# Performance work log

Hardware: AMD Instinct MI355X
Metric: run time of the kernel (lower is better)

## Reference

```python
import jax, jax.numpy as jnp
import numpy as np

# Module hyperparameters (init_kwargs)
NH = 254          # nHidden
NSTEP = 32        # MPC horizon
DT = 1.0 / 60.0   # del_t
EPS = 1e-4
PQ = 5.0
QV = 200.0
QA = 1.0
N_STATE = NH + 2  # hidden embedding + [position, velocity]
NBATCH = 256


def setup_inputs() -> dict:
    key = jax.random.key(0)
    k1, k2, k3, k4, k5, k6 = jax.random.split(key, 6)
    x = jax.random.normal(k1, (NBATCH, NH), dtype=jnp.float32)
    gripper_p = jax.random.normal(k2, (NBATCH,), dtype=jnp.float32)
    own_gripper_v = jax.random.normal(k3, (NBATCH,), dtype=jnp.float32)
    other_gripper_v = jax.random.normal(k4, (NBATCH,), dtype=jnp.float32)
    # Learned parameters (as in __init__): Af ~ U[0,1), Lq = tril(U[0,1))
    Af = jax.random.uniform(k5, (NH, 1), dtype=jnp.float32)
    Lq = jnp.tril(jax.random.uniform(k6, (NH, NH), dtype=jnp.float32))
    return {"x": x, "gripper_p": gripper_p, "own_gripper_v": own_gripper_v,
            "other_gripper_v": other_gripper_v, "Af": Af, "Lq": Lq}


def _mpc_forward(x, gripper_p, own_gripper_v, Af, Lq):
    n = N_STATE
    dt = x.dtype
    eye_n = jnp.eye(n, dtype=dt)

    # ---- Q0: [[Lq Lq^T + eps I, 0], [0, diag(0, Qv)]]  (n x n) ----
    Q0_tl = Lq @ Lq.T + EPS * jnp.eye(NH, dtype=dt)
    Q0 = jnp.zeros((n, n), dt).at[:NH, :NH].set(Q0_tl).at[NH + 1, NH + 1].set(QV)
    w = jnp.ones((NSTEP,), dt).at[-1].set(PQ)        # final-step weight Pq
    Q0_stack = w[:, None, None] * Q0                 # [NSTEP, n, n]
    Q_dia = jax.scipy.linalg.block_diag(*Q0_stack)   # [NSTEP*n, NSTEP*n]

    # ---- A0: [[I, 0, Af], [0, 1, dt], [0, 0, 1]] ----
    A0 = jnp.zeros((n, n), dt)
    A0 = A0.at[:NH, :NH].set(jnp.eye(NH, dtype=dt)).at[:NH, NH + 1].set(Af[:, 0])
    A0 = A0.at[NH, NH].set(1.0).at[NH, NH + 1].set(DT).at[NH + 1, NH + 1].set(1.0)

    # ---- powers A0^1..A0^NSTEP via scan (replaces the Python power loop) ----
    def step(carry, _):
        nxt = carry @ A0
        return nxt, nxt
    _, Pk = jax.lax.scan(step, eye_n, None, length=NSTEP)   # Pk[k] = A0^{k+1}
    P = jnp.concatenate([eye_n[None], Pk], axis=0)          # A0^0 .. A0^NSTEP
    T_ = Pk.reshape(NSTEP * n, n)                           # vstack(A0^1..A0^NSTEP)

    # ---- AN_: block lower-triangular Toeplitz, block (i,j) = A0^{i-j} for j<=i ----
    d = jnp.arange(NSTEP)[:, None] - jnp.arange(NSTEP)[None, :]
    blocks = jnp.where((d >= 0)[:, :, None, None],
                       P[jnp.clip(d, 0, NSTEP)], jnp.zeros((), dt))  # [NSTEP,NSTEP,n,n]
    AN_ = blocks.transpose(0, 2, 1, 3).reshape(NSTEP * n, NSTEP * n)

    B0 = jnp.zeros((n, 1), dt).at[NH, 0].set(0.5 * DT * DT).at[NH + 1, 0].set(DT)
    B_dia = jax.scipy.linalg.block_diag(*jnp.broadcast_to(B0, (NSTEP, n, 1)))

    S_ = AN_ @ B_dia                                        # [NSTEP*n, NSTEP]
    QS = Q_dia @ S_                                         # [NSTEP*n, NSTEP]
    Q_final = 2.0 * (QA * jnp.eye(NSTEP, dtype=dt) + S_.T @ QS) \
              + EPS * jnp.eye(NSTEP, dtype=dt)
    p_final = 2.0 * (T_.T @ QS)                             # [n, NSTEP]

    # ---- batch state x0 = [x, gripper_p, own_gripper_v] ----
    x0 = jnp.concatenate([x, gripper_p[:, None], own_gripper_v[:, None]], axis=1)
    p_x0 = x0 @ p_final                                     # [B, NSTEP]

    # QPFunction with G=0, h=0, no equalities -> unconstrained QP:
    # u = argmin 0.5 u^T Q_final u + p_x0^T u = -Q_final^{-1} p_x0
    u = -jnp.linalg.solve(Q_final, p_x0.T).T                # [B, NSTEP]

    # x_predict = S u + T x0 ; output picks position component (index NH) per step
    x_pred = u @ S_.T + x0 @ T_.T                           # [B, NSTEP*n]
    posi = x_pred.reshape(-1, NSTEP, n)[:, :, NH]           # [B, NSTEP]
    return posi


def reference(x, gripper_p, own_gripper_v, other_gripper_v, Af, Lq):
    # other_gripper_v is accepted but unused in the active forward path (as in source)
    return _mpc_forward(x, gripper_p, own_gripper_v, Af, Lq)
```

## Files before the change

kernel.cpp:

```cpp
#include <hip/hip_runtime.h>

#define NH 254
#define NSTEP 32
#define NB 256

constexpr float  FEPS = 1e-4f;
constexpr double DDT  = 1.0 / 60.0;
constexpr double DQV  = 200.0;
constexpr double DPQ  = 5.0;
constexpr double DQA  = 1.0;
constexpr double DEPS = 1e-4;

__global__ __launch_bounds__(256) void k_fused(const float* __restrict__ Lq,
                                               const float* __restrict__ Af,
                                               const float* __restrict__ x,
                                               const float* __restrict__ gp,
                                               const float* __restrict__ gv,
                                               float* __restrict__ out) {
    __shared__ float  af_sh[256];
    __shared__ float  x_sh[256];
    __shared__ float  t_sh[256];
    __shared__ float  svals[4];
    __shared__ double red[4];
    __shared__ double M[32][34];
    __shared__ double ua[32], ub[32];
    __shared__ float  cA[32], cB[32];

    const int b    = blockIdx.x;
    const int tid  = threadIdx.x;
    const int lane = tid & 63;
    const int wv   = tid >> 6;

    const float gpv = gp[b];
    const float gvv = gv[b];

    af_sh[tid] = (tid < NH) ? Af[tid] : 0.f;
    x_sh[tid]  = (tid < NH) ? x[b * NH + tid] : 0.f;
    __syncthreads();

    {
        float acc = 0.f;
        if (tid < NH) {
            for (int i0 = (tid & ~31); i0 < NH; i0 += 32) {
                float v[32];
                #pragma unroll
                for (int j = 0; j < 32; ++j) {
                    const int i = i0 + j;
                    v[j] = (i < NH) ? Lq[i * NH + tid] : 0.f;
                }
                #pragma unroll
                for (int j = 0; j < 32; ++j)
                    acc += v[j] * af_sh[i0 + j];
            }
        }
        t_sh[tid] = acc;
    }
    __syncthreads();

    {
        float sacc = 0.f;
        for (int r = 0; r < 64; r += 4) {
            float a4[4] = {0.f, 0.f, 0.f, 0.f};
            #pragma unroll
            for (int rr = 0; rr < 4; ++rr) {
                const int i = 64 * wv + r + rr;
                #pragma unroll
                for (int c = 0; c < 4; ++c) {
                    const int kk = lane + 64 * c;
                    const float lv = (i < NH && kk < NH) ? Lq[i * NH + kk] : 0.f;
                    a4[rr] += lv * t_sh[kk];
                }
            }
            #pragma unroll
            for (int rr = 0; rr < 4; ++rr) {
                #pragma unroll
                for (int off = 32; off; off >>= 1)
                    a4[rr] += __shfl_xor(a4[rr], off, 64);
            }
            #pragma unroll
            for (int rr = 0; rr < 4; ++rr) {
                const int i = 64 * wv + r + rr;
                sacc += x_sh[i] * (a4[rr] + FEPS * af_sh[i]);
            }
        }
        if (lane == 0) svals[wv] = sacc;
    }

    {
        double dv = 0.0;
        if (tid < NH) {
            const double td = (double)t_sh[tid];
            const double ad = (double)af_sh[tid];
            dv = td * td + DEPS * ad * ad;
        }
        #pragma unroll
        for (int off = 32; off; off >>= 1) dv += __shfl_xor(dv, off, 64);
        if (lane == 0) red[wv] = dv;
    }
    __syncthreads();
    const double c = red[0] + red[1] + red[2] + red[3];

    for (int e = tid; e < 1024; e += 256) {
        const int j1 = e >> 5, j2 = e & 31;
        const int m = (j1 > j2) ? j1 : j2;
        double s = 0.0;
        for (int kk = m; kk < 32; ++kk) {
            const double wk = (kk == 31) ? DPQ : 1.0;
            s += wk * ((double)(kk - j1) * (double)(kk - j2) * c + DQV);
        }
        M[j1][j2] = 2.0 * DDT * DDT * s + ((j1 == j2) ? (2.0 * DQA + DEPS) : 0.0);
    }
    if (tid < 32) {
        const int j = tid;
        double sa = 0.0, sb = 0.0;
        for (int kk = j; kk < 32; ++kk) {
            const double wk = (kk == 31) ? DPQ : 1.0;
            sa += wk * (double)(kk - j);
            sb += wk * ((double)(kk + 1) * (double)(kk - j) * c + DQV);
        }
        M[j][32] = 2.0 * DDT * sa;
        M[j][33] = 2.0 * DDT * sb;
    }
    __syncthreads();

    {
        const int r   = tid & 31;
        const int cg8 = tid >> 5;
        for (int p = 0; p < 32; ++p) {
            const double f = M[r][p] / M[p][p];
            if (r != p) {
                for (int cc = cg8; cc < 34; cc += 8)
                    if (cc > p) M[r][cc] -= f * M[p][cc];
            }
            __syncthreads();
        }
    }
    if (tid < 32) {
        ua[tid] = -M[tid][32] / M[tid][tid];
        ub[tid] = -M[tid][33] / M[tid][tid];
    }
    __syncthreads();
    if (tid < 32) {
        const int i = tid;
        double ca = 0.0, cb = 0.0;
        for (int j = 0; j <= i; ++j) {
            const double wgt = (double)(i - j) + 0.5;
            ca += wgt * ua[j];
            cb += wgt * ub[j];
        }
        cA[i] = (float)(ca * DDT * DDT);
        cB[i] = (float)((double)(i + 1) * DDT + cb * DDT * DDT);
    }
    __syncthreads();

    if (tid < 32) {
        const float s = svals[0] + svals[1] + svals[2] + svals[3];
        out[b * NSTEP + tid] = gpv + gvv * cB[tid] + s * cA[tid];
    }
}

extern "C" void kernel_launch(void* const* d_in, const int* in_sizes, int n_in,
                              void* d_out, int out_size, void* d_ws, size_t ws_size,
                              hipStream_t stream) {
    const float* x  = (const float*)d_in[0];
    const float* gp = (const float*)d_in[1];
    const float* gv = (const float*)d_in[2];
    const float* Af = (const float*)d_in[4];
    const float* Lq = (const float*)d_in[5];
    float* out = (float*)d_out;

    k_fused<<<NB, 256, 0, stream>>>(Lq, Af, x, gp, gv, out);
}
```

Measured before the change: 106.8 us.

## Split fused kernel into batched Lq^T x product, single solve, and output kernels

The single fused kernel made every batch block recompute t = Lq^T Af and redo the 32x32 double-precision elimination. Now one kernel computes Y = Lq^T x for four batch rows per block (plus t once), one single-block kernel does the solve, and a small kernel combines the results. This removes the per-block duplicate work on Lq and the solve, but adds two kernel launches and a round trip of Y and t through a workspace.

```diff
diff --git a/kernel.cpp b/kernel.cpp
--- a/kernel.cpp
+++ b/kernel.cpp
@@ -11,86 +11,68 @@
 constexpr double DQA  = 1.0;
 constexpr double DEPS = 1e-4;
 
-__global__ __launch_bounds__(256) void k_fused(const float* __restrict__ Lq,
+__global__ __launch_bounds__(256) void k_yt(const float* __restrict__ Lq,
+                                            const float* __restrict__ Af,
+                                            const float* __restrict__ x,
+                                            float* __restrict__ Y,
+                                            float* __restrict__ t_out) {
+    __shared__ float af_sh[256];
+    __shared__ float x_sh[4][256];
+    const int k = threadIdx.x;
+    const int b = blockIdx.x;
+
+    af_sh[k] = (k < NH) ? Af[k] : 0.f;
+    #pragma unroll
+    for (int r = 0; r < 4; ++r) {
+        const int row = 4 * b + r;
+        x_sh[r][k] = (k < NH) ? x[row * NH + k] : 0.f;
+    }
+    __syncthreads();
+
+    float ty = 0.f;
+    float y0 = 0.f, y1 = 0.f, y2 = 0.f, y3 = 0.f;
+    if (k < NH) {
+        for (int i0 = (k & ~31); i0 < NH; i0 += 32) {
+            float v[32];
+            #pragma unroll
+            for (int j = 0; j < 32; ++j) {
+                const int i = i0 + j;
+                v[j] = (i < NH) ? Lq[i * NH + k] : 0.f;
+            }
+            #pragma unroll
+            for (int j = 0; j < 32; ++j) {
+                const int i = i0 + j;
+                ty += v[j] * af_sh[i];
+                y0 += v[j] * x_sh[0][i];
+                y1 += v[j] * x_sh[1][i];
+                y2 += v[j] * x_sh[2][i];
+                y3 += v[j] * x_sh[3][i];
+            }
+        }
+    }
+    Y[(4 * b + 0) * 256 + k] = y0;
+    Y[(4 * b + 1) * 256 + k] = y1;
+    Y[(4 * b + 2) * 256 + k] = y2;
+    Y[(4 * b + 3) * 256 + k] = y3;
+    if (b == 0) t_out[k] = ty;
+}
+
+__global__ __launch_bounds__(256) void k_solve(const float* __restrict__ t_in,
                                                const float* __restrict__ Af,
-                                               const float* __restrict__ x,
-                                               const float* __restrict__ gp,
-                                               const float* __restrict__ gv,
-                                               float* __restrict__ out) {
-    __shared__ float  af_sh[256];
-    __shared__ float  x_sh[256];
-    __shared__ float  t_sh[256];
-    __shared__ float  svals[4];
+                                               float* __restrict__ coef) {
     __shared__ double red[4];
     __shared__ double M[32][34];
     __shared__ double ua[32], ub[32];
-    __shared__ float  cA[32], cB[32];
 
-    const int b    = blockIdx.x;
     const int tid  = threadIdx.x;
     const int lane = tid & 63;
     const int wv   = tid >> 6;
 
-    const float gpv = gp[b];
-    const float gvv = gv[b];
-
-    af_sh[tid] = (tid < NH) ? Af[tid] : 0.f;
-    x_sh[tid]  = (tid < NH) ? x[b * NH + tid] : 0.f;
-    __syncthreads();
-
-    {
-        float acc = 0.f;
-        if (tid < NH) {
-            for (int i0 = (tid & ~31); i0 < NH; i0 += 32) {
-                float v[32];
-                #pragma unroll
-                for (int j = 0; j < 32; ++j) {
-                    const int i = i0 + j;
-                    v[j] = (i < NH) ? Lq[i * NH + tid] : 0.f;
-                }
-                #pragma unroll
-                for (int j = 0; j < 32; ++j)
-                    acc += v[j] * af_sh[i0 + j];
-            }
-        }
-        t_sh[tid] = acc;
-    }
-    __syncthreads();
-
-    {
-        float sacc = 0.f;
-        for (int r = 0; r < 64; r += 4) {
-            float a4[4] = {0.f, 0.f, 0.f, 0.f};
-            #pragma unroll
-            for (int rr = 0; rr < 4; ++rr) {
-                const int i = 64 * wv + r + rr;
-                #pragma unroll
-                for (int c = 0; c < 4; ++c) {
-                    const int kk = lane + 64 * c;
-                    const float lv = (i < NH && kk < NH) ? Lq[i * NH + kk] : 0.f;
-                    a4[rr] += lv * t_sh[kk];
-                }
-            }
-            #pragma unroll
-            for (int rr = 0; rr < 4; ++rr) {
-                #pragma unroll
-                for (int off = 32; off; off >>= 1)
-                    a4[rr] += __shfl_xor(a4[rr], off, 64);
-            }
-            #pragma unroll
-            for (int rr = 0; rr < 4; ++rr) {
-                const int i = 64 * wv + r + rr;
-                sacc += x_sh[i] * (a4[rr] + FEPS * af_sh[i]);
-            }
-        }
-        if (lane == 0) svals[wv] = sacc;
-    }
-
     {
         double dv = 0.0;
         if (tid < NH) {
-            const double td = (double)t_sh[tid];
-            const double ad = (double)af_sh[tid];
+            const double td = (double)t_in[tid];
+            const double ad = (double)Af[tid];
             dv = td * td + DEPS * ad * ad;
         }
         #pragma unroll
@@ -148,15 +130,35 @@
             ca += wgt * ua[j];
             cb += wgt * ub[j];
         }
-        cA[i] = (float)(ca * DDT * DDT);
-        cB[i] = (float)((double)(i + 1) * DDT + cb * DDT * DDT);
+        coef[i]      = (float)(ca * DDT * DDT);
+        coef[32 + i] = (float)((double)(i + 1) * DDT + cb * DDT * DDT);
     }
-    __syncthreads();
+}
 
-    if (tid < 32) {
-        const float s = svals[0] + svals[1] + svals[2] + svals[3];
-        out[b * NSTEP + tid] = gpv + gvv * cB[tid] + s * cA[tid];
+__global__ __launch_bounds__(64) void k_out(const float* __restrict__ x,
+                                            const float* __restrict__ gp,
+                                            const float* __restrict__ gv,
+                                            const float* __restrict__ Af,
+                                            const float* __restrict__ Y,
+                                            const float* __restrict__ t_in,
+                                            const float* __restrict__ coef,
+                                            float* __restrict__ out) {
+    const int b    = blockIdx.x;
+    const int lane = threadIdx.x;
+    float acc = 0.f;
+    #pragma unroll
+    for (int c4 = 0; c4 < 4; ++c4) {
+        const int kk = lane + 64 * c4;
+        const float yv = Y[b * 256 + kk];
+        const float tv = t_in[kk];
+        const float xv = (kk < NH) ? x[b * NH + kk] : 0.f;
+        const float av = (kk < NH) ? Af[kk] : 0.f;
+        acc += yv * tv + FEPS * xv * av;
     }
+    #pragma unroll
+    for (int off = 32; off; off >>= 1) acc += __shfl_xor(acc, off, 64);
+    if (lane < 32)
+        out[b * NSTEP + lane] = gp[b] + gv[b] * coef[32 + lane] + acc * coef[lane];
 }
 
 extern "C" void kernel_launch(void* const* d_in, const int* in_sizes, int n_in,
@@ -169,5 +171,12 @@
     const float* Lq = (const float*)d_in[5];
     float* out = (float*)d_out;
 
-    k_fused<<<NB, 256, 0, stream>>>(Lq, Af, x, gp, gv, out);
+    float* ws   = (float*)d_ws;
+    float* Y    = ws;
+    float* t    = ws + 256 * 256;
+    float* coef = t + 256;
+
+    k_yt   <<<64,  256, 0, stream>>>(Lq, Af, x, Y, t);
+    k_solve<<<1,   256, 0, stream>>>(t, Af, coef);
+    k_out  <<<NB,  64,  0, stream>>>(x, gp, gv, Af, Y, t, coef, out);
 }
```

After: 106.7 us. Within noise of the previous version (-0.1%).
